# Performance work log

Hardware: AMD Instinct MI355X
Metric: run time of the kernel (lower is better)

Reference implementation:

```python
import jax, jax.numpy as jnp
import numpy as np


def setup_inputs() -> dict:
    key = jax.random.key(0)
    k1, k2 = jax.random.split(key)
    decoder_state = jax.random.normal(k1, (64, 1024), dtype=jnp.float32)
    encoder_outputs = jax.random.normal(k2, (64, 2048, 1024), dtype=jnp.float32)
    return {"decoder_state": decoder_state, "encoder_outputs": encoder_outputs}


def reference(decoder_state, encoder_outputs):
    # scores[b, i] = s_t . h_i  -> [B, S]
    scores = jnp.einsum('bh,bsh->bs', decoder_state, encoder_outputs)
    attn_weights = jax.nn.softmax(scores, axis=1)            # [B, S]
    # context[b] = sum_i a[b,i] * h_i -> [B, H]
    context = jnp.einsum('bs,bsh->bh', attn_weights, encoder_outputs)
    return context, attn_weights
```

## Files before the change

### kernel.cpp

```cpp
#include <hip/hip_runtime.h>
#include <math.h>

#define BATCH 64
#define SEQ   2048
#define HID   1024
#define CHUNKS 16
#define ROWS_PER_BLOCK (SEQ / CHUNKS)
#define NWAVES 4
#define ROWS_PER_WAVE (ROWS_PER_BLOCK / NWAVES)
#define PART_STRIDE 1028

typedef float f32x4 __attribute__((ext_vector_type(4)));

__global__ __launch_bounds__(256, 4) void attn_pass1(
    const float* __restrict__ dec, const float* __restrict__ enc,
    float* __restrict__ scores, float* __restrict__ partials)
{
    const int b     = blockIdx.x / CHUNKS;
    const int chunk = blockIdx.x % CHUNKS;
    const int tid   = threadIdx.x;
    const int wave  = tid >> 6;
    const int lane  = tid & 63;

    const f32x4* decv = reinterpret_cast<const f32x4*>(dec + b * HID);
    f32x4 sv[4];
#pragma unroll
    for (int p = 0; p < 4; ++p) sv[p] = decv[p * 64 + lane];

    float m = -1e30f, l = 0.0f;
    f32x4 c[4];
#pragma unroll
    for (int p = 0; p < 4; ++p) c[p] = (f32x4)(0.0f);

    const int row0 = chunk * ROWS_PER_BLOCK + wave * ROWS_PER_WAVE;
    const f32x4* rowp = reinterpret_cast<const f32x4*>(enc + (size_t)b * SEQ * HID)
                        + (size_t)row0 * (HID / 4) + lane;

    f32x4 eA[4], eB[4];
#pragma unroll
    for (int p = 0; p < 4; ++p) eA[p] = __builtin_nontemporal_load(rowp + p * 64);

    auto process = [&](const f32x4 (&e)[4], int r) {
        float dot = 0.f;
#pragma unroll
        for (int p = 0; p < 4; ++p) {
            dot += e[p].x * sv[p].x; dot += e[p].y * sv[p].y;
            dot += e[p].z * sv[p].z; dot += e[p].w * sv[p].w;
        }
#pragma unroll
        for (int off = 32; off > 0; off >>= 1) dot += __shfl_xor(dot, off, 64);

        if (lane == 0) scores[b * SEQ + row0 + r] = dot;

        if (dot <= m) {
            const float pw = __expf(dot - m);
            l += pw;
#pragma unroll
            for (int p = 0; p < 4; ++p) c[p] += pw * e[p];
        } else {
            const float sc = __expf(m - dot);
            l = l * sc + 1.0f;
#pragma unroll
            for (int p = 0; p < 4; ++p) c[p] = c[p] * sc + e[p];
            m = dot;
        }
    };

    for (int r = 0; r < ROWS_PER_WAVE; r += 2) {
        const f32x4* rp1 = rowp + (size_t)(r + 1) * (HID / 4);
#pragma unroll
        for (int p = 0; p < 4; ++p) eB[p] = __builtin_nontemporal_load(rp1 + p * 64);

        process(eA, r);

        if (r + 2 < ROWS_PER_WAVE) {
            const f32x4* rp2 = rowp + (size_t)(r + 2) * (HID / 4);
#pragma unroll
            for (int p = 0; p < 4; ++p) eA[p] = __builtin_nontemporal_load(rp2 + p * 64);
        }

        process(eB, r + 1);
    }

    __shared__ float lm[NWAVES], ll[NWAVES];
    __shared__ float lc[NWAVES][HID];
    f32x4* lcw = reinterpret_cast<f32x4*>(lc[wave]);
#pragma unroll
    for (int p = 0; p < 4; ++p) lcw[p * 64 + lane] = c[p];
    if (lane == 0) { lm[wave] = m; ll[wave] = l; }
    __syncthreads();

    const float M = fmaxf(fmaxf(lm[0], lm[1]), fmaxf(lm[2], lm[3]));
    float w[NWAVES];
    float L = 0.f;
#pragma unroll
    for (int k = 0; k < NWAVES; ++k) { w[k] = __expf(lm[k] - M); L += ll[k] * w[k]; }

    f32x4 acc = (f32x4)(0.0f);
#pragma unroll
    for (int k = 0; k < NWAVES; ++k) {
        f32x4 v = reinterpret_cast<const f32x4*>(lc[k])[tid];
        acc += v * w[k];
    }
    float* rec = partials + (size_t)blockIdx.x * PART_STRIDE;
    reinterpret_cast<f32x4*>(rec)[tid] = acc;
    if (tid == 0) { rec[HID] = M; rec[HID + 1] = L; }
}

__global__ __launch_bounds__(256) void attn_pass2(
    const float* __restrict__ scores, const float* __restrict__ partials,
    float* __restrict__ out_ctx, float* __restrict__ out_attn)
{
    const int b = blockIdx.x;
    const int t = threadIdx.x;

    float mk[CHUNKS], lk[CHUNKS];
    float M = -1e30f;
#pragma unroll
    for (int k = 0; k < CHUNKS; ++k) {
        const float* rec = partials + (size_t)(b * CHUNKS + k) * PART_STRIDE;
        mk[k] = rec[HID];
        lk[k] = rec[HID + 1];
        M = fmaxf(M, mk[k]);
    }
    float L = 0.f;
    float wk[CHUNKS];
#pragma unroll
    for (int k = 0; k < CHUNKS; ++k) { wk[k] = __expf(mk[k] - M); L += lk[k] * wk[k]; }
    const float invL = 1.0f / L;

    f32x4 acc = (f32x4)(0.0f);
#pragma unroll
    for (int k = 0; k < CHUNKS; ++k) {
        const f32x4* rec4 =
            reinterpret_cast<const f32x4*>(partials + (size_t)(b * CHUNKS + k) * PART_STRIDE);
        acc += rec4[t] * wk[k];
    }
    acc *= invL;
    reinterpret_cast<f32x4*>(out_ctx + b * HID)[t] = acc;

    for (int i = t; i < SEQ; i += 256) {
        out_attn[b * SEQ + i] = __expf(scores[b * SEQ + i] - M) * invL;
    }
}

extern "C" void kernel_launch(void* const* d_in, const int* in_sizes, int n_in,
                              void* d_out, int out_size, void* d_ws, size_t ws_size,
                              hipStream_t stream) {
    const float* dec = (const float*)d_in[0];
    const float* enc = (const float*)d_in[1];
    float* out = (float*)d_out;

    float* scores   = (float*)d_ws;
    float* partials = scores + BATCH * SEQ;

    attn_pass1<<<BATCH * CHUNKS, 256, 0, stream>>>(dec, enc, scores, partials);
    attn_pass2<<<BATCH, 256, 0, stream>>>(scores, partials, out, out + BATCH * HID);
}
```

Measured before the change: 100.4 us.

## Fuse combine pass into main kernel via last-block atomic counter

Merges the second (combine) kernel into the first. Each block bumps a per-batch atomic counter, and the last block to finish for a batch performs the cross-chunk softmax merge and writes the outputs. The row prefetch is also deepened from two to four rows in flight, and the dot product is split into four independent accumulators to shorten the dependency chain. This removes a kernel launch and its gap but adds a memset launch, threadfences, and more register pressure from the deeper prefetch.

```diff
diff --git a/kernel.cpp b/kernel.cpp
--- a/kernel.cpp
+++ b/kernel.cpp
@@ -12,9 +12,11 @@
 
 typedef float f32x4 __attribute__((ext_vector_type(4)));
 
-__global__ __launch_bounds__(256, 4) void attn_pass1(
+__global__ __launch_bounds__(256, 4) void attn_fused(
     const float* __restrict__ dec, const float* __restrict__ enc,
-    float* __restrict__ scores, float* __restrict__ partials)
+    float* __restrict__ scores, float* __restrict__ partials,
+    int* __restrict__ counters,
+    float* __restrict__ out_ctx, float* __restrict__ out_attn)
 {
     const int b     = blockIdx.x / CHUNKS;
     const int chunk = blockIdx.x % CHUNKS;
@@ -36,17 +38,21 @@
     const f32x4* rowp = reinterpret_cast<const f32x4*>(enc + (size_t)b * SEQ * HID)
                         + (size_t)row0 * (HID / 4) + lane;
 
-    f32x4 eA[4], eB[4];
+    auto loadrow = [&](f32x4 (&e)[4], int r) {
+        const f32x4* rp = rowp + (size_t)r * (HID / 4);
 #pragma unroll
-    for (int p = 0; p < 4; ++p) eA[p] = __builtin_nontemporal_load(rowp + p * 64);
+        for (int p = 0; p < 4; ++p) e[p] = __builtin_nontemporal_load(rp + p * 64);
+    };
 
     auto process = [&](const f32x4 (&e)[4], int r) {
-        float dot = 0.f;
+        float d0 = e[0].x * sv[0].x, d1 = e[0].y * sv[0].y;
+        float d2 = e[0].z * sv[0].z, d3 = e[0].w * sv[0].w;
 #pragma unroll
-        for (int p = 0; p < 4; ++p) {
-            dot += e[p].x * sv[p].x; dot += e[p].y * sv[p].y;
-            dot += e[p].z * sv[p].z; dot += e[p].w * sv[p].w;
+        for (int p = 1; p < 4; ++p) {
+            d0 += e[p].x * sv[p].x; d1 += e[p].y * sv[p].y;
+            d2 += e[p].z * sv[p].z; d3 += e[p].w * sv[p].w;
         }
+        float dot = (d0 + d1) + (d2 + d3);
 #pragma unroll
         for (int off = 32; off > 0; off >>= 1) dot += __shfl_xor(dot, off, 64);
 
@@ -66,20 +72,14 @@
         }
     };
 
-    for (int r = 0; r < ROWS_PER_WAVE; r += 2) {
-        const f32x4* rp1 = rowp + (size_t)(r + 1) * (HID / 4);
-#pragma unroll
-        for (int p = 0; p < 4; ++p) eB[p] = __builtin_nontemporal_load(rp1 + p * 64);
-
-        process(eA, r);
-
-        if (r + 2 < ROWS_PER_WAVE) {
-            const f32x4* rp2 = rowp + (size_t)(r + 2) * (HID / 4);
-#pragma unroll
-            for (int p = 0; p < 4; ++p) eA[p] = __builtin_nontemporal_load(rp2 + p * 64);
-        }
-
-        process(eB, r + 1);
+    f32x4 e0[4], e1[4], f0[4], f1[4];
+    loadrow(e0, 0); loadrow(e1, 1);
+    loadrow(f0, 2); loadrow(f1, 3);
+    for (int r = 0; r < ROWS_PER_WAVE; r += 4) {
+        process(e0, r); process(e1, r + 1);
+        if (r + 4 < ROWS_PER_WAVE) { loadrow(e0, r + 4); loadrow(e1, r + 5); }
+        process(f0, r + 2); process(f1, r + 3);
+        if (r + 6 < ROWS_PER_WAVE) { loadrow(f0, r + 6); loadrow(f1, r + 7); }
     }
 
     __shared__ float lm[NWAVES], ll[NWAVES];
@@ -105,42 +105,44 @@
     float* rec = partials + (size_t)blockIdx.x * PART_STRIDE;
     reinterpret_cast<f32x4*>(rec)[tid] = acc;
     if (tid == 0) { rec[HID] = M; rec[HID + 1] = L; }
-}
 
-__global__ __launch_bounds__(256) void attn_pass2(
-    const float* __restrict__ scores, const float* __restrict__ partials,
-    float* __restrict__ out_ctx, float* __restrict__ out_attn)
-{
-    const int b = blockIdx.x;
-    const int t = threadIdx.x;
+    __threadfence();
+    __shared__ int is_last;
+    if (tid == 0) {
+        int old = atomicAdd(&counters[b], 1);
+        is_last = (old == CHUNKS - 1);
+    }
+    __syncthreads();
+    if (!is_last) return;
+    __threadfence();
 
     float mk[CHUNKS], lk[CHUNKS];
-    float M = -1e30f;
+    float Mg = -1e30f;
 #pragma unroll
     for (int k = 0; k < CHUNKS; ++k) {
-        const float* rec = partials + (size_t)(b * CHUNKS + k) * PART_STRIDE;
-        mk[k] = rec[HID];
-        lk[k] = rec[HID + 1];
-        M = fmaxf(M, mk[k]);
+        const float* rk = partials + (size_t)(b * CHUNKS + k) * PART_STRIDE;
+        mk[k] = rk[HID];
+        lk[k] = rk[HID + 1];
+        Mg = fmaxf(Mg, mk[k]);
     }
-    float L = 0.f;
+    float Lg = 0.f;
     float wk[CHUNKS];
 #pragma unroll
-    for (int k = 0; k < CHUNKS; ++k) { wk[k] = __expf(mk[k] - M); L += lk[k] * wk[k]; }
-    const float invL = 1.0f / L;
+    for (int k = 0; k < CHUNKS; ++k) { wk[k] = __expf(mk[k] - Mg); Lg += lk[k] * wk[k]; }
+    const float invL = 1.0f / Lg;
 
-    f32x4 acc = (f32x4)(0.0f);
+    f32x4 accg = (f32x4)(0.0f);
 #pragma unroll
     for (int k = 0; k < CHUNKS; ++k) {
-        const f32x4* rec4 =
+        const f32x4* rk4 =
             reinterpret_cast<const f32x4*>(partials + (size_t)(b * CHUNKS + k) * PART_STRIDE);
-        acc += rec4[t] * wk[k];
+        accg += rk4[tid] * wk[k];
     }
-    acc *= invL;
-    reinterpret_cast<f32x4*>(out_ctx + b * HID)[t] = acc;
+    accg *= invL;
+    reinterpret_cast<f32x4*>(out_ctx + b * HID)[tid] = accg;
 
-    for (int i = t; i < SEQ; i += 256) {
-        out_attn[b * SEQ + i] = __expf(scores[b * SEQ + i] - M) * invL;
+    for (int i = tid; i < SEQ; i += 256) {
+        out_attn[b * SEQ + i] = __expf(scores[b * SEQ + i] - Mg) * invL;
     }
 }
 
@@ -153,7 +155,9 @@
 
     float* scores   = (float*)d_ws;
     float* partials = scores + BATCH * SEQ;
+    int*   counters = (int*)(partials + BATCH * CHUNKS * PART_STRIDE);
 
-    attn_pass1<<<BATCH * CHUNKS, 256, 0, stream>>>(dec, enc, scores, partials);
-    attn_pass2<<<BATCH, 256, 0, stream>>>(scores, partials, out, out + BATCH * HID);
+    hipMemsetAsync(counters, 0, BATCH * sizeof(int), stream);
+    attn_fused<<<BATCH * CHUNKS, 256, 0, stream>>>(
+        dec, enc, scores, partials, counters, out, out + BATCH * HID);
 }
```

Result: slower. 397.2 us (+295.5%).
